# Kernel optimization log

Measured on AMD Instinct MI355X. Metric: run time of the kernel, lower is better.

## Reference

```python
import jax, jax.numpy as jnp
import numpy as np

N = 100000
E = 1600000
IN_C = 128
OUT_C = 64
HID = 2 * OUT_C  # 128


def setup_inputs() -> dict:
    key = jax.random.key(0)
    ks = jax.random.split(key, 10)
    s = lambda fan_in: 1.0 / np.sqrt(fan_in)
    inp = {
        "x": jax.random.normal(ks[0], (N, IN_C), dtype=jnp.float32),
        "edge_index": jax.random.randint(ks[1], (2, E), 0, N, dtype=jnp.int64),
        # SAGEConv params: lin_l acts on aggregated neighbors (with bias), lin_r on root (no bias)
        "W1l": jax.random.uniform(ks[2], (IN_C, HID), jnp.float32, -s(IN_C), s(IN_C)),
        "b1": jnp.zeros((HID,), jnp.float32),
        "W1r": jax.random.uniform(ks[3], (IN_C, HID), jnp.float32, -s(IN_C), s(IN_C)),
        "Wml": jax.random.uniform(ks[4], (HID, OUT_C), jnp.float32, -s(HID), s(HID)),
        "bm": jnp.zeros((OUT_C,), jnp.float32),
        "Wmr": jax.random.uniform(ks[5], (HID, OUT_C), jnp.float32, -s(HID), s(HID)),
        "Wsl": jax.random.uniform(ks[6], (HID, OUT_C), jnp.float32, -s(HID), s(HID)),
        "bs": jnp.zeros((OUT_C,), jnp.float32),
        "Wsr": jax.random.uniform(ks[7], (HID, OUT_C), jnp.float32, -s(HID), s(HID)),
    }
    return inp


def _sage_mean(x, src, dst, Wl, b, Wr):
    n = x.shape[0]
    # mean aggregation of source features onto destination nodes
    agg = jax.ops.segment_sum(x[src], dst, num_segments=n)
    cnt = jax.ops.segment_sum(jnp.ones((src.shape[0],), x.dtype), dst, num_segments=n)
    agg = agg / jnp.maximum(cnt, 1.0)[:, None]
    return agg @ Wl + b + x @ Wr


def reference(x, edge_index, W1l, b1, W1r, Wml, bm, Wmr, Wsl, bs, Wsr):
    src, dst = edge_index[0], edge_index[1]
    h = jax.nn.relu(_sage_mean(x, src, dst, W1l, b1, W1r))
    mu = _sage_mean(h, src, dst, Wml, bm, Wmr)
    logstd = _sage_mean(h, src, dst, Wsl, bs, Wsr)
    return mu, logstd
```

## Files before the change

### kernel.cpp

```cpp
#include <hip/hip_runtime.h>


typedef __attribute__((ext_vector_type(8))) short bf16x8;
typedef __attribute__((ext_vector_type(4))) float f32x4;

#define SHIFT 9
#define BW 512

__device__ __forceinline__ unsigned short f2bf(float f) {
    unsigned u = __builtin_bit_cast(unsigned, f);
    u += 0x7fff + ((u >> 16) & 1);
    return (unsigned short)(u >> 16);
}
__device__ __forceinline__ float bflo(unsigned u) { return __builtin_bit_cast(float, u << 16); }
__device__ __forceinline__ float bfhi(unsigned u) { return __builtin_bit_cast(float, u & 0xffff0000u); }

__global__ __launch_bounds__(256) void detect_kernel(const int* __restrict__ raw,
                                                     int* __restrict__ flag, int nCheck) {
    int acc = 0;
    for (int i = blockIdx.x * 256 + threadIdx.x; i < nCheck; i += gridDim.x * 256)
        acc |= raw[2 * i + 1];
    if (acc) atomicOr(flag, 1);
}

__global__ __launch_bounds__(256) void pack_kernel(
    const float* __restrict__ W1l, const float* __restrict__ W1r,
    const float* __restrict__ Wml, const float* __restrict__ Wmr,
    const float* __restrict__ Wsl, const float* __restrict__ Wsr,
    const float* __restrict__ bm, const float* __restrict__ bs,
    unsigned short* __restrict__ B1p, unsigned short* __restrict__ B2p,
    float* __restrict__ bc) {
    int i = blockIdx.x * 256 + threadIdx.x;
    int j = i & 7, lq = (i >> 3) & 63, ks = (i >> 9) & 7, nf = i >> 12;
    int k = ks * 32 + (lq >> 4) * 8 + j;
    int c = nf * 16 + (lq & 15);
    float w1 = (k < 128) ? W1l[k * 128 + c] : W1r[(k - 128) * 128 + c];
    float w2;
    if (k < 128) w2 = (c < 64) ? Wml[k * 64 + c] : Wsl[k * 64 + (c - 64)];
    else         w2 = (c < 64) ? Wmr[(k - 128) * 64 + c] : Wsr[(k - 128) * 64 + (c - 64)];
    B1p[i] = f2bf(w1);
    B2p[i] = f2bf(w2);
    if (i < 128) bc[i] = (i < 64) ? bm[i] : bs[i - 64];
}

__global__ __launch_bounds__(256) void xcvt_kernel(const float* __restrict__ x,
                                                   unsigned short* __restrict__ A1, int total) {
    int i = (blockIdx.x * 256 + threadIdx.x) * 4;
    if (i >= total) return;
    float4 v = *reinterpret_cast<const float4*>(x + i);
    int row = i >> 7, col = i & 127;
    unsigned short* p = A1 + (size_t)row * 256 + 128 + col;
    p[0] = f2bf(v.x); p[1] = f2bf(v.y); p[2] = f2bf(v.z); p[3] = f2bf(v.w);
}

__global__ __launch_bounds__(256) void binA_kernel(
    const int* __restrict__ raw, const int* __restrict__ flag,
    int* __restrict__ bcnt, unsigned* __restrict__ recs, int nE, int cap) {
    __shared__ int cnt[256];
    __shared__ int gbase[256];
    const int t = threadIdx.x;
    const bool is64 = (flag[0] == 0);
    const long long base = (long long)blockIdx.x * 1024;
    cnt[t] = 0;
    __syncthreads();
    int packv[4], loff[4], bk[4];
#pragma unroll
    for (int k = 0; k < 4; ++k) {
        long long e = base + t + k * 256;
        bk[k] = -1;
        if (e < nE) {
            int s, d;
            if (is64) { s = raw[2 * e]; d = raw[2 * (nE + e)]; }
            else      { s = raw[e];     d = raw[nE + e]; }
            bk[k] = d >> SHIFT;
            packv[k] = (s << SHIFT) | (d & (BW - 1));
            loff[k] = atomicAdd(&cnt[bk[k]], 1);
        }
    }
    __syncthreads();
    {
        int c = cnt[t];
        gbase[t] = c ? atomicAdd(&bcnt[t], c) : 0;
    }
    __syncthreads();
#pragma unroll
    for (int k = 0; k < 4; ++k) {
        if (bk[k] >= 0) {
            int pos = gbase[bk[k]] + loff[k];
            if (pos < cap) recs[(size_t)bk[k] * cap + pos] = (unsigned)packv[k];
        }
    }
}

__global__ __launch_bounds__(256) void bscan_kernel(const int* __restrict__ bcnt,
                                                    int* __restrict__ bbase) {
    __shared__ int s[256];
    const int t = threadIdx.x;
    int v = bcnt[t];
    s[t] = v;
    __syncthreads();
    for (int off = 1; off < 256; off <<= 1) {
        int val = (t >= off) ? s[t - off] : 0;
        __syncthreads();
        s[t] += val;
        __syncthreads();
    }
    bbase[t] = s[t] - v;
}

__global__ __launch_bounds__(256) void binB_kernel(
    const unsigned* __restrict__ recs, const int* __restrict__ bcnt,
    const int* __restrict__ bbase, int* __restrict__ rowptr,
    int* __restrict__ csr, int cap, int n, int nE) {
    __shared__ int sdeg[BW];
    __shared__ int scur[BW];
    __shared__ int ssum[256];
    const int b = blockIdx.x;
    const int t = threadIdx.x;
    const int node0 = b << SHIFT;
    int cnt = bcnt[b];
    if (cnt > cap) cnt = cap;
    const int base = bbase[b];
    const unsigned* r = recs + (size_t)b * cap;

    sdeg[t] = 0;
    sdeg[t + 256] = 0;
    __syncthreads();
    for (int i = t; i < cnt; i += 256) atomicAdd(&sdeg[r[i] & (BW - 1)], 1);
    __syncthreads();
    int v0 = sdeg[2 * t], v1 = sdeg[2 * t + 1];
    int sum = v0 + v1;
    ssum[t] = sum;
    __syncthreads();
    for (int off = 1; off < 256; off <<= 1) {
        int val = (t >= off) ? ssum[t - off] : 0;
        __syncthreads();
        ssum[t] += val;
        __syncthreads();
    }
    int ex = ssum[t] - sum;
    scur[2 * t] = ex;
    scur[2 * t + 1] = ex + v0;
    __syncthreads();
#pragma unroll
    for (int q = 0; q < 2; ++q) {
        int i = t + q * 256;
        int node = node0 + i;
        if (node < n) rowptr[node] = base + scur[i];
    }
    if (b == gridDim.x - 1 && t == 0) rowptr[n] = nE;
    __syncthreads();
    for (int i = t; i < cnt; i += 256) {
        unsigned rec = r[i];
        int pos = base + atomicAdd(&scur[rec & (BW - 1)], 1);
        csr[pos] = (int)(rec >> SHIFT);
    }
}

__global__ __launch_bounds__(256) void gather_kernel(const unsigned int* __restrict__ feat,
                                                     const int* __restrict__ rowptr,
                                                     const int* __restrict__ csr,
                                                     unsigned int* __restrict__ agg, int n) {
    int wv = (blockIdx.x * 256 + threadIdx.x) >> 6;
    if (wv >= n) return;
    int lane = threadIdx.x & 63;
    int eg = lane >> 4;
    int c4 = (lane & 15) * 4;
    int beg = rowptr[wv], end = rowptr[wv + 1];
    float acc[8] = {0.f, 0.f, 0.f, 0.f, 0.f, 0.f, 0.f, 0.f};
    int jb = beg;
    for (; jb + 8 <= end; jb += 8) {
        int s0 = csr[jb + eg];
        int s1 = csr[jb + 4 + eg];
        uint4 v0 = *reinterpret_cast<const uint4*>(feat + (size_t)s0 * 128 + c4);
        uint4 v1 = *reinterpret_cast<const uint4*>(feat + (size_t)s1 * 128 + c4);
        acc[0] += bflo(v0.x); acc[1] += bfhi(v0.x);
        acc[2] += bflo(v0.y); acc[3] += bfhi(v0.y);
        acc[4] += bflo(v0.z); acc[5] += bfhi(v0.z);
        acc[6] += bflo(v0.w); acc[7] += bfhi(v0.w);
        acc[0] += bflo(v1.x); acc[1] += bfhi(v1.x);
        acc[2] += bflo(v1.y); acc[3] += bfhi(v1.y);
        acc[4] += bflo(v1.z); acc[5] += bfhi(v1.z);
        acc[6] += bflo(v1.w); acc[7] += bfhi(v1.w);
    }
    for (; jb < end; jb += 4) {
        int e = jb + eg;
        bool ok = e < end;
        int s = csr[ok ? e : beg];
        uint4 v = *reinterpret_cast<const uint4*>(feat + (size_t)s * 128 + c4);
        if (ok) {
            acc[0] += bflo(v.x); acc[1] += bfhi(v.x);
            acc[2] += bflo(v.y); acc[3] += bfhi(v.y);
            acc[4] += bflo(v.z); acc[5] += bfhi(v.z);
            acc[6] += bflo(v.w); acc[7] += bfhi(v.w);
        }
    }
#pragma unroll
    for (int q = 0; q < 8; ++q) {
        acc[q] += __shfl_xor(acc[q], 16);
        acc[q] += __shfl_xor(acc[q], 32);
    }
    if (eg == 0) {
        float ic = 1.0f / fmaxf((float)(end - beg), 1.0f);
        uint4 r;
        r.x = (unsigned)f2bf(acc[0] * ic) | ((unsigned)f2bf(acc[1] * ic) << 16);
        r.y = (unsigned)f2bf(acc[2] * ic) | ((unsigned)f2bf(acc[3] * ic) << 16);
        r.z = (unsigned)f2bf(acc[4] * ic) | ((unsigned)f2bf(acc[5] * ic) << 16);
        r.w = (unsigned)f2bf(acc[6] * ic) | ((unsigned)f2bf(acc[7] * ic) << 16);
        *reinterpret_cast<uint4*>(agg + (size_t)wv * 128 + c4) = r;
    }
}

template <int MODE>
__global__ __launch_bounds__(256) void mfma_gemm(const unsigned short* __restrict__ A,
                                                 const unsigned short* __restrict__ Bp,
                                                 const float* __restrict__ bias,
                                                 void* __restrict__ outp, int n) {
    const int tid = threadIdx.x;
    const int w = tid >> 6, l = tid & 63;
    const int lr = l & 15;
    const int lg = l >> 4;
    const int row0 = blockIdx.x * 128 + w * 32;

    f32x4 acc[2][8];
#pragma unroll
    for (int mf = 0; mf < 2; ++mf)
#pragma unroll
        for (int nf = 0; nf < 8; ++nf) acc[mf][nf] = (f32x4)(0.0f);

    int r0 = row0 + lr;       if (r0 > n - 1) r0 = n - 1;
    int r1 = row0 + 16 + lr;  if (r1 > n - 1) r1 = n - 1;
    const unsigned short* a0p = A + (size_t)r0 * 256 + lg * 8;
    const unsigned short* a1p = A + (size_t)r1 * 256 + lg * 8;
    const unsigned short* bp = Bp + (size_t)l * 8;

    for (int ks = 0; ks < 8; ++ks) {
        bf16x8 a0 = *reinterpret_cast<const bf16x8*>(a0p + ks * 32);
        bf16x8 a1 = *reinterpret_cast<const bf16x8*>(a1p + ks * 32);
#pragma unroll
        for (int nf = 0; nf < 8; ++nf) {
            bf16x8 b = *reinterpret_cast<const bf16x8*>(bp + ((nf * 8 + ks) << 9));
            acc[0][nf] = __builtin_amdgcn_mfma_f32_16x16x32_bf16(a0, b, acc[0][nf], 0, 0, 0);
            acc[1][nf] = __builtin_amdgcn_mfma_f32_16x16x32_bf16(a1, b, acc[1][nf], 0, 0, 0);
        }
    }

    float bv[8];
#pragma unroll
    for (int nf = 0; nf < 8; ++nf) bv[nf] = bias[nf * 16 + lr];

#pragma unroll
    for (int mf = 0; mf < 2; ++mf)
#pragma unroll
        for (int j = 0; j < 4; ++j) {
            int row = row0 + mf * 16 + lg * 4 + j;
            if (row >= n) continue;
#pragma unroll
            for (int nf = 0; nf < 8; ++nf) {
                int col = nf * 16 + lr;
                float v = acc[mf][nf][j] + bv[nf];
                if (MODE == 0) {
                    v = fmaxf(v, 0.0f);
                    ((unsigned short*)outp)[(size_t)row * 256 + 128 + col] = f2bf(v);
                } else {
                    float* o = (float*)outp;
                    if (col < 64) o[(size_t)row * 64 + col] = v;
                    else o[(size_t)n * 64 + (size_t)row * 64 + (col - 64)] = v;
                }
            }
        }
}

extern "C" void kernel_launch(void* const* d_in, const int* in_sizes, int n_in,
                              void* d_out, int out_size, void* d_ws, size_t ws_size,
                              hipStream_t stream) {
    const float* x = (const float*)d_in[0];
    const int* eidx_raw = (const int*)d_in[1];
    const float* W1l = (const float*)d_in[2];
    const float* b1 = (const float*)d_in[3];
    const float* W1r = (const float*)d_in[4];
    const float* Wml = (const float*)d_in[5];
    const float* bm = (const float*)d_in[6];
    const float* Wmr = (const float*)d_in[7];
    const float* Wsl = (const float*)d_in[8];
    const float* bs = (const float*)d_in[9];
    const float* Wsr = (const float*)d_in[10];
    float* out = (float*)d_out;

    const int n = in_sizes[0] / 128;
    const int nE = in_sizes[1] / 2;

    const int NB = ((n - 1) >> SHIFT) + 1;
    long long capll = (((long long)nE << SHIFT) / n) * 5 / 4 + 1024;
    const int cap = (int)((capll + 15) & ~15LL);

    char* ws = (char*)d_ws;
    const size_t a_bytes = (size_t)n * 512;
    const size_t a1_off = 0;
    const size_t a2_off = a1_off + a_bytes;
    const size_t recs_off = a2_off;
    const size_t csr_off = a2_off + a_bytes;
    const size_t rowptr_off = csr_off + (size_t)nE * 4;
    const size_t bcnt_off = rowptr_off + (size_t)(n + 1) * 4;
    const size_t flag_off = bcnt_off + 1024;
    const size_t bbase_off = flag_off + 4;
    const size_t b1p_off = (bbase_off + 1024 + 255) & ~(size_t)255;
    const size_t b2p_off = b1p_off + 65536;
    const size_t bc_off = b2p_off + 65536;

    unsigned short* A1 = (unsigned short*)(ws + a1_off);
    unsigned short* A2 = (unsigned short*)(ws + a2_off);
    unsigned* recs = (unsigned*)(ws + recs_off);
    int* csr = (int*)(ws + csr_off);
    int* rowptr = (int*)(ws + rowptr_off);
    int* bcnt = (int*)(ws + bcnt_off);
    int* flag = (int*)(ws + flag_off);
    int* bbase = (int*)(ws + bbase_off);
    unsigned short* B1p = (unsigned short*)(ws + b1p_off);
    unsigned short* B2p = (unsigned short*)(ws + b2p_off);
    float* bc = (float*)(ws + bc_off);

    hipMemsetAsync(bcnt, 0, 1024 + 4, stream);

    const int nCheck = nE < 65536 ? nE : 65536;
    detect_kernel<<<64, 256, 0, stream>>>(eidx_raw, flag, nCheck);
    pack_kernel<<<128, 256, 0, stream>>>(W1l, W1r, Wml, Wmr, Wsl, Wsr, bm, bs, B1p, B2p, bc);
    xcvt_kernel<<<(n * 128 / 4 + 255) / 256, 256, 0, stream>>>(x, A1, n * 128);

    binA_kernel<<<(nE + 1023) / 1024, 256, 0, stream>>>(eidx_raw, flag, bcnt, recs, nE, cap);
    bscan_kernel<<<1, 256, 0, stream>>>(bcnt, bbase);
    binB_kernel<<<NB, 256, 0, stream>>>(recs, bcnt, bbase, rowptr, csr, cap, n, nE);

    const int gather_blocks = (n * 64 + 255) / 256;
    const int gemm_blocks = (n + 127) / 128;

    gather_kernel<<<gather_blocks, 256, 0, stream>>>(
        (const unsigned int*)A1 + 64, rowptr, csr, (unsigned int*)A1, n);
    mfma_gemm<0><<<gemm_blocks, 256, 0, stream>>>(A1, B1p, b1, A2, n);

    gather_kernel<<<gather_blocks, 256, 0, stream>>>(
        (const unsigned int*)A2 + 64, rowptr, csr, (unsigned int*)A2, n);
    mfma_gemm<1><<<gemm_blocks, 256, 0, stream>>>(A2, B2p, bc, out, n);
}
```

Before: 305.9 us.

## Pad CSR rows to multiples of four, fuse prep kernels, inline bucket scan

Each node's CSR row is padded to a multiple of four, and the pad slots point to an extra zero row appended to the feature buffers. This lets the gather loop run without a masked tail and with a software-pipelined, prefetched load. The detect, pack and convert kernels merge into one prep launch, and the separate bucket scan kernel is folded into binB, where every block recomputes the scan. This removes launches and tail divergence, at the cost of extra CSR memory, padded loads of the zero row, and a redundant scan in each binB block.

```diff
diff --git a/kernel.cpp b/kernel.cpp
--- a/kernel.cpp
+++ b/kernel.cpp
@@ -3,6 +3,7 @@
 
 typedef __attribute__((ext_vector_type(8))) short bf16x8;
 typedef __attribute__((ext_vector_type(4))) float f32x4;
+typedef __attribute__((ext_vector_type(2))) float f32x2;
 
 #define SHIFT 9
 #define BW 512
@@ -15,42 +16,49 @@
 __device__ __forceinline__ float bflo(unsigned u) { return __builtin_bit_cast(float, u << 16); }
 __device__ __forceinline__ float bfhi(unsigned u) { return __builtin_bit_cast(float, u & 0xffff0000u); }
 
-__global__ __launch_bounds__(256) void detect_kernel(const int* __restrict__ raw,
-                                                     int* __restrict__ flag, int nCheck) {
-    int acc = 0;
-    for (int i = blockIdx.x * 256 + threadIdx.x; i < nCheck; i += gridDim.x * 256)
-        acc |= raw[2 * i + 1];
-    if (acc) atomicOr(flag, 1);
-}
-
-__global__ __launch_bounds__(256) void pack_kernel(
+__global__ __launch_bounds__(256) void prep_kernel(
+    const float* __restrict__ x, const int* __restrict__ raw, int* __restrict__ flag,
     const float* __restrict__ W1l, const float* __restrict__ W1r,
     const float* __restrict__ Wml, const float* __restrict__ Wmr,
     const float* __restrict__ Wsl, const float* __restrict__ Wsr,
     const float* __restrict__ bm, const float* __restrict__ bs,
     unsigned short* __restrict__ B1p, unsigned short* __restrict__ B2p,
-    float* __restrict__ bc) {
-    int i = blockIdx.x * 256 + threadIdx.x;
-    int j = i & 7, lq = (i >> 3) & 63, ks = (i >> 9) & 7, nf = i >> 12;
-    int k = ks * 32 + (lq >> 4) * 8 + j;
-    int c = nf * 16 + (lq & 15);
-    float w1 = (k < 128) ? W1l[k * 128 + c] : W1r[(k - 128) * 128 + c];
-    float w2;
-    if (k < 128) w2 = (c < 64) ? Wml[k * 64 + c] : Wsl[k * 64 + (c - 64)];
-    else         w2 = (c < 64) ? Wmr[(k - 128) * 64 + c] : Wsr[(k - 128) * 64 + (c - 64)];
-    B1p[i] = f2bf(w1);
-    B2p[i] = f2bf(w2);
-    if (i < 128) bc[i] = (i < 64) ? bm[i] : bs[i - 64];
-}
-
-__global__ __launch_bounds__(256) void xcvt_kernel(const float* __restrict__ x,
-                                                   unsigned short* __restrict__ A1, int total) {
-    int i = (blockIdx.x * 256 + threadIdx.x) * 4;
-    if (i >= total) return;
-    float4 v = *reinterpret_cast<const float4*>(x + i);
-    int row = i >> 7, col = i & 127;
-    unsigned short* p = A1 + (size_t)row * 256 + 128 + col;
-    p[0] = f2bf(v.x); p[1] = f2bf(v.y); p[2] = f2bf(v.z); p[3] = f2bf(v.w);
+    float* __restrict__ bc, unsigned short* __restrict__ A1,
+    unsigned short* __restrict__ A2, int n, int nE, int nXB) {
+    const int b = blockIdx.x;
+    const int t = threadIdx.x;
+    if (b < nXB) {
+        int i = (b * 256 + t) * 4;
+        if (i < n * 128) {
+            float4 v = *reinterpret_cast<const float4*>(x + i);
+            int row = i >> 7, col = i & 127;
+            unsigned short* p = A1 + (size_t)row * 256 + 128 + col;
+            p[0] = f2bf(v.x); p[1] = f2bf(v.y); p[2] = f2bf(v.z); p[3] = f2bf(v.w);
+        }
+    } else if (b < nXB + 64) {
+        const int nCheck = nE < 65536 ? nE : 65536;
+        int acc = 0;
+        for (int i = (b - nXB) * 256 + t; i < nCheck; i += 64 * 256)
+            acc |= raw[2 * i + 1];
+        if (acc) atomicOr(flag, 1);
+    } else if (b < nXB + 192) {
+        int i = (b - nXB - 64) * 256 + t;
+        int j = i & 7, lq = (i >> 3) & 63, ks = (i >> 9) & 7, nf = i >> 12;
+        int k = ks * 32 + (lq >> 4) * 8 + j;
+        int c = nf * 16 + (lq & 15);
+        float w1 = (k < 128) ? W1l[k * 128 + c] : W1r[(k - 128) * 128 + c];
+        float w2;
+        if (k < 128) w2 = (c < 64) ? Wml[k * 64 + c] : Wsl[k * 64 + (c - 64)];
+        else         w2 = (c < 64) ? Wmr[(k - 128) * 64 + c] : Wsr[(k - 128) * 64 + (c - 64)];
+        B1p[i] = f2bf(w1);
+        B2p[i] = f2bf(w2);
+        if (i < 128) bc[i] = (i < 64) ? bm[i] : bs[i - 64];
+    } else {
+        if (t < 64) {
+            ((unsigned*)A1)[(size_t)n * 128 + 64 + t] = 0;
+            ((unsigned*)A2)[(size_t)n * 128 + 64 + t] = 0;
+        }
+    }
 }
 
 __global__ __launch_bounds__(256) void binA_kernel(
@@ -92,45 +100,19 @@
     }
 }
 
-__global__ __launch_bounds__(256) void bscan_kernel(const int* __restrict__ bcnt,
-                                                    int* __restrict__ bbase) {
-    __shared__ int s[256];
-    const int t = threadIdx.x;
-    int v = bcnt[t];
-    s[t] = v;
-    __syncthreads();
-    for (int off = 1; off < 256; off <<= 1) {
-        int val = (t >= off) ? s[t - off] : 0;
-        __syncthreads();
-        s[t] += val;
-        __syncthreads();
-    }
-    bbase[t] = s[t] - v;
-}
-
 __global__ __launch_bounds__(256) void binB_kernel(
     const unsigned* __restrict__ recs, const int* __restrict__ bcnt,
-    const int* __restrict__ bbase, int* __restrict__ rowptr,
-    int* __restrict__ csr, int cap, int n, int nE) {
+    int* __restrict__ rowptrP, int* __restrict__ cnts,
+    int* __restrict__ csr, int cap, int n, int NB) {
     __shared__ int sdeg[BW];
     __shared__ int scur[BW];
     __shared__ int ssum[256];
     const int b = blockIdx.x;
     const int t = threadIdx.x;
     const int node0 = b << SHIFT;
-    int cnt = bcnt[b];
-    if (cnt > cap) cnt = cap;
-    const int base = bbase[b];
-    const unsigned* r = recs + (size_t)b * cap;
-
-    sdeg[t] = 0;
-    sdeg[t + 256] = 0;
-    __syncthreads();
-    for (int i = t; i < cnt; i += 256) atomicAdd(&sdeg[r[i] & (BW - 1)], 1);
-    __syncthreads();
-    int v0 = sdeg[2 * t], v1 = sdeg[2 * t + 1];
-    int sum = v0 + v1;
-    ssum[t] = sum;
+
+    int rawb = (t < NB) ? bcnt[t] : 0;
+    ssum[t] = rawb;
     __syncthreads();
     for (int off = 1; off < 256; off <<= 1) {
         int val = (t >= off) ? ssum[t - off] : 0;
@@ -138,27 +120,64 @@
         ssum[t] += val;
         __syncthreads();
     }
+    const int base = ((b == 0) ? 0 : ssum[b - 1]) + b * 3 * BW;
+    int cnt = bcnt[b];
+    if (cnt > cap) cnt = cap;
+    const unsigned* r = recs + (size_t)b * cap;
+    __syncthreads();
+
+    sdeg[t] = 0;
+    sdeg[t + 256] = 0;
+    __syncthreads();
+    for (int i = t; i < cnt; i += 256) atomicAdd(&sdeg[r[i] & (BW - 1)], 1);
+    __syncthreads();
+    int d0 = sdeg[2 * t], d1 = sdeg[2 * t + 1];
+    int p0 = (d0 + 3) & ~3, p1 = (d1 + 3) & ~3;
+    int sum = p0 + p1;
+    ssum[t] = sum;
+    __syncthreads();
+    for (int off = 1; off < 256; off <<= 1) {
+        int val = (t >= off) ? ssum[t - off] : 0;
+        __syncthreads();
+        ssum[t] += val;
+        __syncthreads();
+    }
     int ex = ssum[t] - sum;
     scur[2 * t] = ex;
-    scur[2 * t + 1] = ex + v0;
+    scur[2 * t + 1] = ex + p0;
     __syncthreads();
 #pragma unroll
     for (int q = 0; q < 2; ++q) {
-        int i = t + q * 256;
+        int i = 2 * t + q;
         int node = node0 + i;
-        if (node < n) rowptr[node] = base + scur[i];
-    }
-    if (b == gridDim.x - 1 && t == 0) rowptr[n] = nE;
+        if (node < n) {
+            rowptrP[node] = base + scur[i];
+            cnts[node] = sdeg[i];
+        }
+    }
     __syncthreads();
     for (int i = t; i < cnt; i += 256) {
         unsigned rec = r[i];
         int pos = base + atomicAdd(&scur[rec & (BW - 1)], 1);
         csr[pos] = (int)(rec >> SHIFT);
     }
+    __syncthreads();
+#pragma unroll
+    for (int q = 0; q < 2; ++q) {
+        int i = 2 * t + q;
+        int node = node0 + i;
+        if (node < n) {
+            int d = sdeg[i];
+            int pad = (4 - (d & 3)) & 3;
+            int st = base + scur[i];
+            for (int k = 0; k < pad; ++k) csr[st + k] = n;
+        }
+    }
 }
 
 __global__ __launch_bounds__(256) void gather_kernel(const unsigned int* __restrict__ feat,
-                                                     const int* __restrict__ rowptr,
+                                                     const int* __restrict__ rowptrP,
+                                                     const int* __restrict__ cnts,
                                                      const int* __restrict__ csr,
                                                      unsigned int* __restrict__ agg, int n) {
     int wv = (blockIdx.x * 256 + threadIdx.x) >> 6;
@@ -166,42 +185,37 @@
     int lane = threadIdx.x & 63;
     int eg = lane >> 4;
     int c4 = (lane & 15) * 4;
-    int beg = rowptr[wv], end = rowptr[wv + 1];
-    float acc[8] = {0.f, 0.f, 0.f, 0.f, 0.f, 0.f, 0.f, 0.f};
+    int beg = rowptrP[wv];
+    int deg = cnts[wv];
+    int endp = beg + ((deg + 3) & ~3);
+    f32x2 a0 = (f32x2)(0.f), a1 = (f32x2)(0.f), a2 = (f32x2)(0.f), a3 = (f32x2)(0.f);
     int jb = beg;
-    for (; jb + 8 <= end; jb += 8) {
-        int s0 = csr[jb + eg];
-        int s1 = csr[jb + 4 + eg];
-        uint4 v0 = *reinterpret_cast<const uint4*>(feat + (size_t)s0 * 128 + c4);
-        uint4 v1 = *reinterpret_cast<const uint4*>(feat + (size_t)s1 * 128 + c4);
-        acc[0] += bflo(v0.x); acc[1] += bfhi(v0.x);
-        acc[2] += bflo(v0.y); acc[3] += bfhi(v0.y);
-        acc[4] += bflo(v0.z); acc[5] += bfhi(v0.z);
-        acc[6] += bflo(v0.w); acc[7] += bfhi(v0.w);
-        acc[0] += bflo(v1.x); acc[1] += bfhi(v1.x);
-        acc[2] += bflo(v1.y); acc[3] += bfhi(v1.y);
-        acc[4] += bflo(v1.z); acc[5] += bfhi(v1.z);
-        acc[6] += bflo(v1.w); acc[7] += bfhi(v1.w);
-    }
-    for (; jb < end; jb += 4) {
-        int e = jb + eg;
-        bool ok = e < end;
-        int s = csr[ok ? e : beg];
+    if (jb < endp) {
+        int s = csr[jb + eg];
         uint4 v = *reinterpret_cast<const uint4*>(feat + (size_t)s * 128 + c4);
-        if (ok) {
-            acc[0] += bflo(v.x); acc[1] += bfhi(v.x);
-            acc[2] += bflo(v.y); acc[3] += bfhi(v.y);
-            acc[4] += bflo(v.z); acc[5] += bfhi(v.z);
-            acc[6] += bflo(v.w); acc[7] += bfhi(v.w);
-        }
-    }
+#pragma unroll 2
+        for (jb += 4; jb < endp; jb += 4) {
+            int s2 = csr[jb + eg];
+            uint4 v2 = *reinterpret_cast<const uint4*>(feat + (size_t)s2 * 128 + c4);
+            a0 += (f32x2){bflo(v.x), bfhi(v.x)};
+            a1 += (f32x2){bflo(v.y), bfhi(v.y)};
+            a2 += (f32x2){bflo(v.z), bfhi(v.z)};
+            a3 += (f32x2){bflo(v.w), bfhi(v.w)};
+            v = v2;
+        }
+        a0 += (f32x2){bflo(v.x), bfhi(v.x)};
+        a1 += (f32x2){bflo(v.y), bfhi(v.y)};
+        a2 += (f32x2){bflo(v.z), bfhi(v.z)};
+        a3 += (f32x2){bflo(v.w), bfhi(v.w)};
+    }
+    float acc[8] = {a0.x, a0.y, a1.x, a1.y, a2.x, a2.y, a3.x, a3.y};
 #pragma unroll
     for (int q = 0; q < 8; ++q) {
         acc[q] += __shfl_xor(acc[q], 16);
         acc[q] += __shfl_xor(acc[q], 32);
     }
     if (eg == 0) {
-        float ic = 1.0f / fmaxf((float)(end - beg), 1.0f);
+        float ic = 1.0f / fmaxf((float)deg, 1.0f);
         uint4 r;
         r.x = (unsigned)f2bf(acc[0] * ic) | ((unsigned)f2bf(acc[1] * ic) << 16);
         r.y = (unsigned)f2bf(acc[2] * ic) | ((unsigned)f2bf(acc[3] * ic) << 16);
@@ -293,18 +307,19 @@
     const int NB = ((n - 1) >> SHIFT) + 1;
     long long capll = (((long long)nE << SHIFT) / n) * 5 / 4 + 1024;
     const int cap = (int)((capll + 15) & ~15LL);
+    const int csr_ints = nE + NB * 3 * BW + 64;
 
     char* ws = (char*)d_ws;
-    const size_t a_bytes = (size_t)n * 512;
+    const size_t a_bytes = (size_t)(n + 1) * 512;
     const size_t a1_off = 0;
     const size_t a2_off = a1_off + a_bytes;
     const size_t recs_off = a2_off;
     const size_t csr_off = a2_off + a_bytes;
-    const size_t rowptr_off = csr_off + (size_t)nE * 4;
-    const size_t bcnt_off = rowptr_off + (size_t)(n + 1) * 4;
+    const size_t rowptr_off = csr_off + (size_t)csr_ints * 4;
+    const size_t cnts_off = rowptr_off + (size_t)n * 4;
+    const size_t bcnt_off = cnts_off + (size_t)n * 4;
     const size_t flag_off = bcnt_off + 1024;
-    const size_t bbase_off = flag_off + 4;
-    const size_t b1p_off = (bbase_off + 1024 + 255) & ~(size_t)255;
+    const size_t b1p_off = (flag_off + 4 + 255) & ~(size_t)255;
     const size_t b2p_off = b1p_off + 65536;
     const size_t bc_off = b2p_off + 65536;
 
@@ -312,33 +327,32 @@
     unsigned short* A2 = (unsigned short*)(ws + a2_off);
     unsigned* recs = (unsigned*)(ws + recs_off);
     int* csr = (int*)(ws + csr_off);
-    int* rowptr = (int*)(ws + rowptr_off);
+    int* rowptrP = (int*)(ws + rowptr_off);
+    int* cnts = (int*)(ws + cnts_off);
     int* bcnt = (int*)(ws + bcnt_off);
     int* flag = (int*)(ws + flag_off);
-    int* bbase = (int*)(ws + bbase_off);
     unsigned short* B1p = (unsigned short*)(ws + b1p_off);
     unsigned short* B2p = (unsigned short*)(ws + b2p_off);
     float* bc = (float*)(ws + bc_off);
 
     hipMemsetAsync(bcnt, 0, 1024 + 4, stream);
 
-    const int nCheck = nE < 65536 ? nE : 65536;
-    detect_kernel<<<64, 256, 0, stream>>>(eidx_raw, flag, nCheck);
-    pack_kernel<<<128, 256, 0, stream>>>(W1l, W1r, Wml, Wmr, Wsl, Wsr, bm, bs, B1p, B2p, bc);
-    xcvt_kernel<<<(n * 128 / 4 + 255) / 256, 256, 0, stream>>>(x, A1, n * 128);
+    const int nXB = (n * 32 + 255) / 256;
+    prep_kernel<<<nXB + 193, 256, 0, stream>>>(x, eidx_raw, flag, W1l, W1r, Wml, Wmr,
+                                               Wsl, Wsr, bm, bs, B1p, B2p, bc, A1, A2,
+                                               n, nE, nXB);
 
     binA_kernel<<<(nE + 1023) / 1024, 256, 0, stream>>>(eidx_raw, flag, bcnt, recs, nE, cap);
-    bscan_kernel<<<1, 256, 0, stream>>>(bcnt, bbase);
-    binB_kernel<<<NB, 256, 0, stream>>>(recs, bcnt, bbase, rowptr, csr, cap, n, nE);
+    binB_kernel<<<NB, 256, 0, stream>>>(recs, bcnt, rowptrP, cnts, csr, cap, n, NB);
 
     const int gather_blocks = (n * 64 + 255) / 256;
     const int gemm_blocks = (n + 127) / 128;
 
     gather_kernel<<<gather_blocks, 256, 0, stream>>>(
-        (const unsigned int*)A1 + 64, rowptr, csr, (unsigned int*)A1, n);
+        (const unsigned int*)A1 + 64, rowptrP, cnts, csr, (unsigned int*)A1, n);
     mfma_gemm<0><<<gemm_blocks, 256, 0, stream>>>(A1, B1p, b1, A2, n);
 
     gather_kernel<<<gather_blocks, 256, 0, stream>>>(
-        (const unsigned int*)A2 + 64, rowptr, csr, (unsigned int*)A2, n);
+        (const unsigned int*)A2 + 64, rowptrP, cnts, csr, (unsigned int*)A2, n);
     mfma_gemm<1><<<gemm_blocks, 256, 0, stream>>>(A2, B2p, bc, out, n);
 }
```

Result: faster. 287.9 us (-5.9%).
